# Kernel tuning notes

Measured on AMD Instinct MI355X. Metric: run time of the kernel, lower is better.

Reference implementation:

```python
import jax, jax.numpy as jnp
import numpy as np

VAR_CXCY = 0.1   # SSD encoding variances
VAR_WH = 0.2
THRESH = 0.5     # match threshold from forward()
EPS = 1e-6


def point_form(p):
    """[P,4] (cx,cy,w,h) -> (x1,y1,x2,y2)."""
    return jnp.concatenate([p[..., :2] - p[..., 2:] / 2,
                            p[..., :2] + p[..., 2:] / 2], axis=-1)


def iou(a, b):
    """a: [N,4] xyxy, b: [P,4] xyxy -> [N,P] jaccard overlap."""
    lt = jnp.maximum(a[:, None, :2], b[None, :, :2])
    rb = jnp.minimum(a[:, None, 2:], b[None, :, 2:])
    wh = jnp.clip(rb - lt, 0.0)
    inter = wh[..., 0] * wh[..., 1]
    area_a = (a[:, 2] - a[:, 0]) * (a[:, 3] - a[:, 1])
    area_b = (b[:, 2] - b[:, 0]) * (b[:, 3] - b[:, 1])
    return inter / (area_a[:, None] + area_b[None, :] - inter + EPS)


def match_one(gt, labels, priors, priors_pt):
    """SSD match for a single image.
    gt: [N,4] xyxy, labels: [N] int, priors: [P,4] cxcywh, priors_pt: [P,4] xyxy.
    Returns loc targets [P,4] and conf targets [P] (0 = background).
    """
    ov = iou(gt, priors_pt)                       # [N,P]
    best_prior_idx = jnp.argmax(ov, axis=1)        # [N] best prior per gt
    best_truth_ov = jnp.max(ov, axis=0)            # [P]
    best_truth_idx = jnp.argmax(ov, axis=0)        # [P] best gt per prior
    n = gt.shape[0]
    # ensure every gt keeps its best prior
    best_truth_ov = best_truth_ov.at[best_prior_idx].set(2.0)
    best_truth_idx = best_truth_idx.at[best_prior_idx].set(jnp.arange(n))
    matches = gt[best_truth_idx]                   # [P,4]
    conf = labels[best_truth_idx] + 1              # shift so 0 = background
    conf = jnp.where(best_truth_ov < THRESH, 0, conf)
    # encode matched boxes relative to priors
    m_cxcy = (matches[:, :2] + matches[:, 2:]) * 0.5
    m_wh = jnp.clip(matches[:, 2:] - matches[:, :2], EPS)
    g_cxcy = (m_cxcy - priors[:, :2]) / (VAR_CXCY * priors[:, 2:])
    g_wh = jnp.log(m_wh / priors[:, 2:]) / VAR_WH
    return jnp.concatenate([g_cxcy, g_wh], axis=1), conf


def setup_inputs() -> dict:
    key = jax.random.key(0)
    k1, k2, k3, k4, k5 = jax.random.split(key, 5)
    B, N, P = 32, 100, 8732
    # ground-truth boxes: valid xyxy corners in [0,1]
    xy1 = jax.random.uniform(k1, (B, N, 2)) * 0.7
    wh = 0.05 + jax.random.uniform(k2, (B, N, 2)) * 0.25
    gt_boxes = jnp.concatenate([xy1, xy1 + wh], axis=-1).astype(jnp.float32)
    gt_labels = jax.random.randint(k3, (B, N), 0, 20)
    # priors: cxcywh
    p_cxcy = jax.random.uniform(k4, (P, 2))
    p_wh = 0.05 + jax.random.uniform(k5, (P, 2)) * 0.45
    priors = jnp.concatenate([p_cxcy, p_wh], axis=-1).astype(jnp.float32)
    return {"gt_boxes": gt_boxes, "gt_labels": gt_labels, "priors": priors}


def reference(gt_boxes, gt_labels, priors):
    priors_pt = point_form(priors)
    loc_t, conf_t = jax.vmap(
        lambda g, l: match_one(g, l, priors, priors_pt))(gt_boxes, gt_labels)
    return loc_t, conf_t
```

## Files before the change

kernel.cpp:

```cpp
#include <hip/hip_runtime.h>

#pragma clang fp contract(off)

#define BB 32
#define NN 100
#define PP 8732
#define CH 16
#define LDW 257

__global__ __launch_bounds__(256) void k_iou_pass(
    const float* __restrict__ gt,
    const float* __restrict__ priors,
    unsigned long long* __restrict__ gkey,
    unsigned char* __restrict__ m8)
{
    __shared__ unsigned int s_iou[CH * LDW];
    __shared__ unsigned long long s_part[NN][17];

    const int b = blockIdx.y;
    const int t = threadIdx.x;
    const int p = blockIdx.x * 256 + t;
    const bool valid = p < PP;
    const int pc = valid ? p : (PP - 1);

    const float4 pr = reinterpret_cast<const float4*>(priors)[pc];
    const float px1 = pr.x - pr.z * 0.5f;
    const float py1 = pr.y - pr.w * 0.5f;
    const float px2 = pr.x + pr.z * 0.5f;
    const float py2 = pr.y + pr.w * 0.5f;
    const float area_b = (px2 - px1) * (py2 - py1);

    const float4* __restrict__ gtb =
        reinterpret_cast<const float4*>(gt) + b * NN;

    float best_ov = -1.0f;
    int best_j = 0;

    for (int jc = 0; jc < NN; jc += CH) {
        const int nr = (NN - jc) < CH ? (NN - jc) : CH;

        #pragma unroll 4
        for (int jj = 0; jj < nr; ++jj) {
            float4 g = gtb[jc + jj];
            float area_a = (g.z - g.x) * (g.w - g.y);
            float ltx = fmaxf(g.x, px1), lty = fmaxf(g.y, py1);
            float rbx = fminf(g.z, px2), rby = fminf(g.w, py2);
            float w = fmaxf(rbx - ltx, 0.0f), h = fmaxf(rby - lty, 0.0f);
            float inter = w * h;
            float iou = inter / (area_a + area_b - inter + 1e-6f);
            if (!valid) iou = 0.0f;
            if (iou > best_ov) { best_ov = iou; best_j = jc + jj; }
            s_iou[jj * LDW + t] = __float_as_uint(iou);
        }
        __syncthreads();

        {
            const int r = t & 15;
            const int s = t >> 4;
            if (r < nr) {
                const unsigned int* row = s_iou + r * LDW + s * 16;
                unsigned int bb = row[0];
                int bi = 0;
                #pragma unroll
                for (int i = 1; i < 16; ++i) {
                    unsigned int v = row[i];
                    if (v > bb) { bb = v; bi = i; }
                }
                int pw = blockIdx.x * 256 + s * 16 + bi;
                s_part[jc + r][s] = ((unsigned long long)bb << 32) |
                                    (unsigned int)(~pw);
            }
        }
        __syncthreads();
    }

    if (t < NN) {
        unsigned long long best = s_part[t][0];
        #pragma unroll
        for (int s = 1; s < 16; ++s) {
            unsigned long long k = s_part[t][s];
            if (k > best) best = k;
        }
        atomicMax(&gkey[b * NN + t], best);
    }
    if (valid) {
        m8[b * PP + p] =
            (unsigned char)(best_j | ((best_ov < 0.5f) ? 0x80 : 0));
    }
}

__global__ __launch_bounds__(256) void k_encode(
    const float* __restrict__ gt,
    const int*   __restrict__ labels,
    const float* __restrict__ priors,
    const unsigned long long* __restrict__ gkey,
    const unsigned char* __restrict__ m8,
    float* __restrict__ loc_out,
    float* __restrict__ conf_out)
{
    __shared__ int s_forced[256];

    const int b = blockIdx.y;
    const int t = threadIdx.x;
    const int p = blockIdx.x * 256 + t;

    s_forced[t] = -1;
    __syncthreads();
    if (t < NN) {
        int kp = (int)~(unsigned int)(gkey[b * NN + t] & 0xFFFFFFFFull);
        int lp = kp - blockIdx.x * 256;
        if ((unsigned)lp < 256u) atomicMax(&s_forced[lp], t);
    }
    __syncthreads();

    if (p >= PP) return;
    const int forced_j = s_forced[t];

    const unsigned char m = m8[b * PP + p];
    const int j    = (forced_j >= 0) ? forced_j : (m & 0x7f);
    const int lab  = labels[b * NN + j];
    const int conf = (forced_j < 0 && (m & 0x80)) ? 0 : (lab + 1);

    const float4 pr = reinterpret_cast<const float4*>(priors)[p];
    const float4 g  = reinterpret_cast<const float4*>(gt)[b * NN + j];
    const float mcx = (g.x + g.z) * 0.5f;
    const float mcy = (g.y + g.w) * 0.5f;
    const float mw  = fmaxf(g.z - g.x, 1e-6f);
    const float mh  = fmaxf(g.w - g.y, 1e-6f);
    const float gcx = (mcx - pr.x) / (0.1f * pr.z);
    const float gcy = (mcy - pr.y) / (0.1f * pr.w);
    const float gw  = logf(mw / pr.z) / 0.2f;
    const float gh  = logf(mh / pr.w) / 0.2f;

    reinterpret_cast<float4*>(loc_out)[b * PP + p] =
        make_float4(gcx, gcy, gw, gh);
    conf_out[b * PP + p] = (float)conf;
}

extern "C" void kernel_launch(void* const* d_in, const int* in_sizes, int n_in,
                              void* d_out, int out_size, void* d_ws, size_t ws_size,
                              hipStream_t stream) {
    const float* gt     = (const float*)d_in[0];
    const int*   labels = (const int*)  d_in[1];
    const float* priors = (const float*)d_in[2];

    float* loc  = (float*)d_out;
    float* conf = (float*)d_out + (size_t)BB * PP * 4;

    unsigned long long* gkey = (unsigned long long*)d_ws;
    unsigned char* m8 = (unsigned char*)d_ws + (size_t)BB * NN * 8;

    hipMemsetAsync(gkey, 0, (size_t)BB * NN * 8, stream);

    dim3 grid((PP + 255) / 256, BB);
    k_iou_pass<<<grid, 256, 0, stream>>>(gt, priors, gkey, m8);
    k_encode<<<grid, 256, 0, stream>>>(gt, labels, priors, gkey, m8, loc, conf);
}
```

Before: 99.74 us.

## Fuse IoU and encode kernels using a per-image grid barrier

Merges the IoU/argmax pass and the encode pass into one kernel. Blocks belonging to the same image count themselves on an atomic counter and spin until all 35 have arrived, then read the per-gt best-prior keys. Each thread keeps its best match and overlap in registers, so the byte matrix no longer goes through global memory and one launch is removed. The spin barrier relies on all 35 blocks of an image being co-resident, which the occupancy hint of 5 blocks per SIMD is meant to help guarantee; if they are not, it can deadlock or stall.

```diff
diff --git a/kernel.cpp b/kernel.cpp
--- a/kernel.cpp
+++ b/kernel.cpp
@@ -7,15 +7,20 @@
 #define PP 8732
 #define CH 16
 #define LDW 257
+#define NBX 35
 
-__global__ __launch_bounds__(256) void k_iou_pass(
+__global__ __launch_bounds__(256, 5) void k_fused(
     const float* __restrict__ gt,
+    const int*   __restrict__ labels,
     const float* __restrict__ priors,
     unsigned long long* __restrict__ gkey,
-    unsigned char* __restrict__ m8)
+    unsigned int* __restrict__ done,
+    float* __restrict__ loc_out,
+    float* __restrict__ conf_out)
 {
     __shared__ unsigned int s_iou[CH * LDW];
     __shared__ unsigned long long s_part[NN][17];
+    int* s_forced = (int*)s_iou;
 
     const int b = blockIdx.y;
     const int t = threadIdx.x;
@@ -83,46 +88,34 @@
         }
         atomicMax(&gkey[b * NN + t], best);
     }
-    if (valid) {
-        m8[b * PP + p] =
-            (unsigned char)(best_j | ((best_ov < 0.5f) ? 0x80 : 0));
+    __threadfence();
+    __syncthreads();
+
+    if (t == 0) {
+        if (atomicAdd(&done[b], 1u) + 1u < (unsigned)NBX) {
+            while (atomicAdd(&done[b], 0u) < (unsigned)NBX)
+                __builtin_amdgcn_s_sleep(2);
+        }
     }
-}
-
-__global__ __launch_bounds__(256) void k_encode(
-    const float* __restrict__ gt,
-    const int*   __restrict__ labels,
-    const float* __restrict__ priors,
-    const unsigned long long* __restrict__ gkey,
-    const unsigned char* __restrict__ m8,
-    float* __restrict__ loc_out,
-    float* __restrict__ conf_out)
-{
-    __shared__ int s_forced[256];
-
-    const int b = blockIdx.y;
-    const int t = threadIdx.x;
-    const int p = blockIdx.x * 256 + t;
+    __syncthreads();
 
     s_forced[t] = -1;
     __syncthreads();
     if (t < NN) {
-        int kp = (int)~(unsigned int)(gkey[b * NN + t] & 0xFFFFFFFFull);
+        unsigned long long k = atomicAdd(&gkey[b * NN + t], 0ull);
+        int kp = (int)~(unsigned int)(k & 0xFFFFFFFFull);
         int lp = kp - blockIdx.x * 256;
         if ((unsigned)lp < 256u) atomicMax(&s_forced[lp], t);
     }
     __syncthreads();
 
-    if (p >= PP) return;
+    if (!valid) return;
     const int forced_j = s_forced[t];
+    const int j    = (forced_j >= 0) ? forced_j : best_j;
+    const int lab  = labels[b * NN + j];
+    const int conf = (forced_j < 0 && best_ov < 0.5f) ? 0 : (lab + 1);
 
-    const unsigned char m = m8[b * PP + p];
-    const int j    = (forced_j >= 0) ? forced_j : (m & 0x7f);
-    const int lab  = labels[b * NN + j];
-    const int conf = (forced_j < 0 && (m & 0x80)) ? 0 : (lab + 1);
-
-    const float4 pr = reinterpret_cast<const float4*>(priors)[p];
-    const float4 g  = reinterpret_cast<const float4*>(gt)[b * NN + j];
+    const float4 g = reinterpret_cast<const float4*>(gt)[b * NN + j];
     const float mcx = (g.x + g.z) * 0.5f;
     const float mcy = (g.y + g.w) * 0.5f;
     const float mw  = fmaxf(g.z - g.x, 1e-6f);
@@ -148,11 +141,11 @@
     float* conf = (float*)d_out + (size_t)BB * PP * 4;
 
     unsigned long long* gkey = (unsigned long long*)d_ws;
-    unsigned char* m8 = (unsigned char*)d_ws + (size_t)BB * NN * 8;
+    unsigned int* done = (unsigned int*)((char*)d_ws + (size_t)BB * NN * 8);
 
-    hipMemsetAsync(gkey, 0, (size_t)BB * NN * 8, stream);
+    hipMemsetAsync(d_ws, 0, (size_t)BB * NN * 8 + BB * 4, stream);
 
-    dim3 grid((PP + 255) / 256, BB);
-    k_iou_pass<<<grid, 256, 0, stream>>>(gt, priors, gkey, m8);
-    k_encode<<<grid, 256, 0, stream>>>(gt, labels, priors, gkey, m8, loc, conf);
+    dim3 grid(NBX, BB);
+    k_fused<<<grid, 256, 0, stream>>>(gt, labels, priors, gkey, done,
+                                      loc, conf);
 }
```

Measured after the change: 182.2 us. +82.6%, slower.

## Replace memset and global atomics with per-block partials reduced in encode

Applied to the files above, without the earlier changes.

The IoU pass now writes each block's per-ground-truth best prior key into a partial buffer. The encode kernel reduces those 35 partials per image, which removes the workspace memset and the global 64-bit atomicMax whenever the workspace is large enough. Ground-truth areas are precomputed once per block in shared memory, the inner loop is fully unrolled, and the per-iteration validity masking is dropped. The cost is more global reads in each encode block. Correctness for the out-of-range padded threads now depends on the tie-breaking order of the packed key.

```diff
diff --git a/kernel.cpp b/kernel.cpp
--- a/kernel.cpp
+++ b/kernel.cpp
@@ -7,21 +7,32 @@
 #define PP 8732
 #define CH 16
 #define LDW 257
+#define NBX 35
 
+template <bool USE_PART>
 __global__ __launch_bounds__(256) void k_iou_pass(
     const float* __restrict__ gt,
     const float* __restrict__ priors,
-    unsigned long long* __restrict__ gkey,
+    unsigned long long* __restrict__ red,
     unsigned char* __restrict__ m8)
 {
     __shared__ unsigned int s_iou[CH * LDW];
     __shared__ unsigned long long s_part[NN][17];
+    __shared__ float s_area[NN];
 
     const int b = blockIdx.y;
     const int t = threadIdx.x;
     const int p = blockIdx.x * 256 + t;
     const bool valid = p < PP;
     const int pc = valid ? p : (PP - 1);
+
+    const float4* __restrict__ gtb =
+        reinterpret_cast<const float4*>(gt) + b * NN;
+
+    if (t < NN) {
+        float4 g = gtb[t];
+        s_area[t] = (g.z - g.x) * (g.w - g.y);
+    }
 
     const float4 pr = reinterpret_cast<const float4*>(priors)[pc];
     const float px1 = pr.x - pr.z * 0.5f;
@@ -30,25 +41,24 @@
     const float py2 = pr.y + pr.w * 0.5f;
     const float area_b = (px2 - px1) * (py2 - py1);
 
-    const float4* __restrict__ gtb =
-        reinterpret_cast<const float4*>(gt) + b * NN;
-
     float best_ov = -1.0f;
     int best_j = 0;
+
+    __syncthreads();
 
     for (int jc = 0; jc < NN; jc += CH) {
         const int nr = (NN - jc) < CH ? (NN - jc) : CH;
 
-        #pragma unroll 4
-        for (int jj = 0; jj < nr; ++jj) {
+        #pragma unroll
+        for (int jj = 0; jj < CH; ++jj) {
+            if (jj >= nr) break;
             float4 g = gtb[jc + jj];
-            float area_a = (g.z - g.x) * (g.w - g.y);
+            float area_a = s_area[jc + jj];
             float ltx = fmaxf(g.x, px1), lty = fmaxf(g.y, py1);
             float rbx = fminf(g.z, px2), rby = fminf(g.w, py2);
             float w = fmaxf(rbx - ltx, 0.0f), h = fmaxf(rby - lty, 0.0f);
             float inter = w * h;
             float iou = inter / (area_a + area_b - inter + 1e-6f);
-            if (!valid) iou = 0.0f;
             if (iou > best_ov) { best_ov = iou; best_j = jc + jj; }
             s_iou[jj * LDW + t] = __float_as_uint(iou);
         }
@@ -81,7 +91,11 @@
             unsigned long long k = s_part[t][s];
             if (k > best) best = k;
         }
-        atomicMax(&gkey[b * NN + t], best);
+        if (USE_PART) {
+            red[((size_t)b * NBX + blockIdx.x) * NN + t] = best;
+        } else {
+            atomicMax(&red[b * NN + t], best);
+        }
     }
     if (valid) {
         m8[b * PP + p] =
@@ -89,11 +103,12 @@
     }
 }
 
+template <bool USE_PART>
 __global__ __launch_bounds__(256) void k_encode(
     const float* __restrict__ gt,
     const int*   __restrict__ labels,
     const float* __restrict__ priors,
-    const unsigned long long* __restrict__ gkey,
+    const unsigned long long* __restrict__ red,
     const unsigned char* __restrict__ m8,
     float* __restrict__ loc_out,
     float* __restrict__ conf_out)
@@ -107,7 +122,19 @@
     s_forced[t] = -1;
     __syncthreads();
     if (t < NN) {
-        int kp = (int)~(unsigned int)(gkey[b * NN + t] & 0xFFFFFFFFull);
+        unsigned long long best;
+        if (USE_PART) {
+            const unsigned long long* q = red + (size_t)b * NBX * NN + t;
+            best = q[0];
+            #pragma unroll 5
+            for (int bx = 1; bx < NBX; ++bx) {
+                unsigned long long k = q[(size_t)bx * NN];
+                if (k > best) best = k;
+            }
+        } else {
+            best = red[b * NN + t];
+        }
+        int kp = (int)~(unsigned int)(best & 0xFFFFFFFFull);
         int lp = kp - blockIdx.x * 256;
         if ((unsigned)lp < 256u) atomicMax(&s_forced[lp], t);
     }
@@ -147,12 +174,22 @@
     float* loc  = (float*)d_out;
     float* conf = (float*)d_out + (size_t)BB * PP * 4;
 
-    unsigned long long* gkey = (unsigned long long*)d_ws;
-    unsigned char* m8 = (unsigned char*)d_ws + (size_t)BB * NN * 8;
+    const size_t part_bytes = (size_t)BB * NBX * NN * 8;
+    const size_t m8_bytes   = (size_t)BB * PP;
+    dim3 grid(NBX, BB);
 
-    hipMemsetAsync(gkey, 0, (size_t)BB * NN * 8, stream);
-
-    dim3 grid((PP + 255) / 256, BB);
-    k_iou_pass<<<grid, 256, 0, stream>>>(gt, priors, gkey, m8);
-    k_encode<<<grid, 256, 0, stream>>>(gt, labels, priors, gkey, m8, loc, conf);
+    if (ws_size >= part_bytes + m8_bytes) {
+        unsigned long long* part = (unsigned long long*)d_ws;
+        unsigned char* m8 = (unsigned char*)d_ws + part_bytes;
+        k_iou_pass<true><<<grid, 256, 0, stream>>>(gt, priors, part, m8);
+        k_encode<true><<<grid, 256, 0, stream>>>(gt, labels, priors, part,
+                                                 m8, loc, conf);
+    } else {
+        unsigned long long* gkey = (unsigned long long*)d_ws;
+        unsigned char* m8 = (unsigned char*)d_ws + (size_t)BB * NN * 8;
+        hipMemsetAsync(gkey, 0, (size_t)BB * NN * 8, stream);
+        k_iou_pass<false><<<grid, 256, 0, stream>>>(gt, priors, gkey, m8);
+        k_encode<false><<<grid, 256, 0, stream>>>(gt, labels, priors, gkey,
+                                                  m8, loc, conf);
+    }
 }
```

Result: faster. 96.60 us (-3.1%).
